# Kernel optimization log

Measured on AMD Instinct MI355X. Metric: run time of the kernel, lower is better.

## Reference

```python
import jax, jax.numpy as jnp
import numpy as np

# Dims: B=batch, C=n_car, N=n_node, E=embed_dim, H=n_heads
B, C, N, E = 64, 8, 512, 512
H = 8
CLIP = 10.0


def setup_inputs() -> dict:
    key = jax.random.key(0)
    ks = jax.random.split(key, 12)
    s = 1.0 / np.sqrt(E)
    mask = jax.random.bernoulli(ks[10], 0.3, (B, C, 1, N))
    mask = mask.at[..., 0].set(False)  # ensure at least one unmasked node per (b,c)
    return {
        "node_embeddings": jax.random.normal(ks[0], (B, N, E), jnp.float32),
        "graph_embedding": jax.random.normal(ks[1], (B, E), jnp.float32),
        "step_context": jax.random.normal(ks[2], (B, C, 1, E + 2), jnp.float32),
        "mask": mask,
        "Wk1": jax.random.normal(ks[3], (E, E), jnp.float32) * s,
        "Wv": jax.random.normal(ks[4], (E, E), jnp.float32) * s,
        "Wk2": jax.random.normal(ks[5], (E, E), jnp.float32) * s,
        "Wq_fixed": jax.random.normal(ks[6], (E, E), jnp.float32) * s,
        "Wout": jax.random.normal(ks[7], (E, E), jnp.float32) * s,
        "Wq_step": jax.random.normal(ks[8], (E, E + 2), jnp.float32) * s,
        "v": jax.random.uniform(ks[9], (E,), jnp.float32, -s, s),
    }


def reference(node_embeddings, graph_embedding, step_context, mask,
              Wk1, Wv, Wk2, Wq_fixed, Wout, Wq_step, v):
    dh = E // H
    neg = jnp.asarray(-1e9, node_embeddings.dtype)

    # compute_static: projections (torch Linear: x @ W.T). K/V/Q_fixed are
    # broadcast over the car dim instead of materialized via .repeat (same math).
    Q_fixed = (graph_embedding @ Wq_fixed.T)[:, None, None, :]  # [B,1,1,E]
    K1 = node_embeddings @ Wk1.T                                 # [B,N,E]
    V = node_embeddings @ Wv.T                                   # [B,N,E]
    K2 = node_embeddings @ Wk2.T                                 # [B,N,E]

    # compute_dynamic
    Q_step = step_context @ Wq_step.T                            # [B,C,1,E]
    Q1 = Q_fixed + Q_step                                        # [B,C,1,E]

    # MHA (need_W=False): split heads, masked scaled dot-product, merge heads.
    qh = Q1.reshape(B, C, H, dh)                                 # q-len 1 squeezed
    kh = K1.reshape(B, N, H, dh)
    vh = V.reshape(B, N, H, dh)
    scores = jnp.einsum('bchd,bnhd->bchn', qh, kh) * (1.0 / np.sqrt(dh))
    m = mask[:, :, 0, :][:, :, None, :]                          # [B,C,1,N]
    scores = jnp.where(m, neg, scores)
    attn = jax.nn.softmax(scores, axis=-1)
    heads = jnp.einsum('bchn,bnhd->bchd', attn, vh).reshape(B, C, E)
    Q3 = heads @ Wout.T                                          # [B,C,E] (Q2.squeeze(2))

    # Pointer logits (SHA): u = tanh(Q_fixed+Q_step) @ v, repeated over E,
    # dotted with K2 => u_scalar * sum_e K2, then tanh-clipped and masked.
    u_scalar = jnp.einsum('bcqe,e->bcq', jnp.tanh(Q1), v)        # [B,C,1]
    k2sum = K2.sum(-1)                                           # [B,N]
    raw = u_scalar * k2sum[:, None, :]                           # [B,C,N]
    logits = CLIP * jnp.tanh(raw * (1.0 / np.sqrt(E)))
    logits = jnp.where(mask[:, :, 0, :], neg, logits)
    logits = logits.reshape(B, C * N)                            # view(batch, -1)
    return logits, Q3
```

## Files before the change

kernel.cpp:

```cpp
#include <hip/hip_runtime.h>


typedef _Float16 f16x8 __attribute__((ext_vector_type(8)));
typedef float f32x4 __attribute__((ext_vector_type(4)));

__device__ __forceinline__ void async16(const void* g, void* l) {
  __builtin_amdgcn_global_load_lds(
      (const __attribute__((address_space(1))) unsigned int*)g,
      (__attribute__((address_space(3))) unsigned int*)l, 16, 0, 0);
}

__device__ __forceinline__ float fast_tanh(float x) {
  float ax = fabsf(x);
  float t = __expf(-2.f * ax);
  float r = (1.f - t) / (1.f + t);
  return copysignf(r, x);
}

__global__ __launch_bounds__(256) void prep_q1(
    const float* __restrict__ Wk1, const float* __restrict__ Wv,
    const float* __restrict__ Wk2, _Float16* __restrict__ W1h,
    _Float16* __restrict__ W2h, float* __restrict__ colsum,
    const float* __restrict__ ge, const float* __restrict__ sc,
    const float* __restrict__ Wqf, const float* __restrict__ Wqs,
    float* __restrict__ Q1) {
  const int bid = blockIdx.x;
  if (bid < 272) {
    if (bid < 16) {
      const int tx = threadIdx.x & 31, ty = threadIdx.x >> 5;
      const int col = bid * 32 + tx;
      float s = 0.f;
#pragma unroll 4
      for (int e = ty * 64; e < ty * 64 + 64; ++e) s += Wk2[e * 512 + col];
      __shared__ float red[8][32];
      red[ty][tx] = s;
      __syncthreads();
      if (ty == 0) {
        float t = 0.f;
#pragma unroll
        for (int g = 0; g < 8; ++g) t += red[g][tx];
        colsum[col] = t;
      }
    } else {
      const int cb = bid - 16;
      const float* src = (cb < 128) ? Wk1 : Wv;
      _Float16* dst = (cb < 128) ? W1h : W2h;
      const size_t off = (size_t)(cb & 127) * 2048 + threadIdx.x * 8;
      float4 a = *(const float4*)(src + off);
      float4 b = *(const float4*)(src + off + 4);
      union { _Float16 h[8]; uint4 u; } pk;
      pk.h[0] = (_Float16)a.x; pk.h[1] = (_Float16)a.y;
      pk.h[2] = (_Float16)a.z; pk.h[3] = (_Float16)a.w;
      pk.h[4] = (_Float16)b.x; pk.h[5] = (_Float16)b.y;
      pk.h[6] = (_Float16)b.z; pk.h[7] = (_Float16)b.w;
      *(uint4*)(dst + off) = pk.u;
    }
    return;
  }

  const int b2 = bid - 272;
  const int mb = b2 & 7, nb = (b2 >> 3) & 7, ks = b2 >> 6;
  const int tid = threadIdx.x;
  const int lane = tid & 63, wave = tid >> 6;
  const int wm = (wave >> 1) * 32, wn = (wave & 1) * 32;

  __shared__ __align__(16) _Float16 As[64][40];
  __shared__ __align__(16) _Float16 Ws[64][40];

  f32x4 acc[2][2] = {};
  const int qd = (lane >> 4) * 8, rr = lane & 15;

  for (int kt = 0; kt < 9; ++kt) {
    const int kb = ks * 288 + kt * 32;
#pragma unroll
    for (int f0 = 0; f0 < 2; ++f0) {
      int f = tid + f0 * 256;
      int r = f >> 3, c4 = (f & 7) * 4;
      int m = mb * 64 + r;
      int e = nb * 64 + r;
#pragma unroll
      for (int j = 0; j < 4; ++j) {
        int k = kb + c4 + j;
        float a = 0.f, w = 0.f;
        if (k < 512) {
          a = ge[(m >> 3) * 512 + k];
          w = Wqf[(size_t)e * 512 + k];
        } else if (k < 1026) {
          a = sc[(size_t)m * 514 + (k - 512)];
          w = Wqs[(size_t)e * 514 + (k - 512)];
        }
        As[r][c4 + j] = (_Float16)a;
        Ws[r][c4 + j] = (_Float16)w;
      }
    }
    __syncthreads();
    f16x8 af[2], bfr[2];
#pragma unroll
    for (int mi = 0; mi < 2; ++mi) af[mi] = *(const f16x8*)&As[wm + mi * 16 + rr][qd];
#pragma unroll
    for (int ni = 0; ni < 2; ++ni) bfr[ni] = *(const f16x8*)&Ws[wn + ni * 16 + rr][qd];
#pragma unroll
    for (int mi = 0; mi < 2; ++mi)
#pragma unroll
      for (int ni = 0; ni < 2; ++ni)
        acc[mi][ni] =
            __builtin_amdgcn_mfma_f32_16x16x32_f16(af[mi], bfr[ni], acc[mi][ni], 0, 0, 0);
    __syncthreads();
  }

  const int col = lane & 15, rq = (lane >> 4) * 4;
#pragma unroll
  for (int mi = 0; mi < 2; ++mi)
#pragma unroll
    for (int ni = 0; ni < 2; ++ni)
#pragma unroll
      for (int r = 0; r < 4; ++r) {
        int m = mb * 64 + wm + mi * 16 + rq + r;
        int e = nb * 64 + wn + ni * 16 + col;
        atomicAdd(&Q1[(size_t)m * 512 + e], acc[mi][ni][r]);
      }
}

__global__ __launch_bounds__(256, 2) void gemm_kv(
    const float* __restrict__ A, const _Float16* __restrict__ W1,
    const _Float16* __restrict__ W2, const float* __restrict__ colsum,
    _Float16* __restrict__ K1, _Float16* __restrict__ Vt,
    float* __restrict__ k2sum) {
  const int flat = (int)(blockIdx.y * 4 + blockIdx.x);
  const int work = (flat & 7) * 128 + (flat >> 3);
  const int nb = work & 3;
  const int mb = work >> 2;
  const int tid = threadIdx.x, lane = tid & 63, wave = tid >> 6;
  const int wm = (wave >> 1) * 64, wn = (wave & 1) * 64;
  const int row0 = mb * 128, col0 = nb * 128;
  const int b = mb >> 2;

  __shared__ __align__(16) _Float16 Ah[128 * 64];
  __shared__ __align__(16) _Float16 Wb[2][2][128 * 64];

  f32x4 acc1[4][4] = {}, acc2[4][4] = {};
  float k2p[4] = {0.f, 0.f, 0.f, 0.f};
  const int q = lane >> 4, rr = lane & 15;
  const int wlr = lane >> 3, wlc = lane & 7;
  const int cswz = wlc ^ wlr;

  const int ar0 = tid >> 3, ac = tid & 7;
  const float* aptr = A + (size_t)(row0 + ar0) * 512 + ac * 8;
  const int aslot = ac ^ (ar0 & 7);

  float4 areg[4][2];
  float4 cs0, cs1;

  auto issue_a = [&](int kt) {
#pragma unroll
    for (int j = 0; j < 4; ++j) {
      const float* gp = aptr + (size_t)j * 32 * 512 + kt * 64;
      areg[j][0] = *(const float4*)gp;
      areg[j][1] = *(const float4*)(gp + 4);
    }
    if (nb == 0) {
      const float* csp = colsum + kt * 64 + ac * 8;
      cs0 = *(const float4*)csp;
      cs1 = *(const float4*)(csp + 4);
    }
  };
  auto issue_w = [&](int kt, int buf) {
    const int kbase = kt * 64;
#pragma unroll
    for (int j = 0; j < 4; ++j) {
      int r = wave * 32 + j * 8 + wlr;
      int ldsrow = (wave * 32 + j * 8) * 64;
      size_t goff = (size_t)(col0 + r) * 512 + kbase + cswz * 8;
      async16(W1 + goff, &Wb[buf][0][ldsrow]);
      async16(W2 + goff, &Wb[buf][1][ldsrow]);
    }
  };
  auto write_a = [&](int kt) {
#pragma unroll
    for (int j = 0; j < 4; ++j) {
      union { _Float16 h[8]; uint4 u; } pk;
      float4 lo = areg[j][0], hi = areg[j][1];
      pk.h[0] = (_Float16)lo.x; pk.h[1] = (_Float16)lo.y;
      pk.h[2] = (_Float16)lo.z; pk.h[3] = (_Float16)lo.w;
      pk.h[4] = (_Float16)hi.x; pk.h[5] = (_Float16)hi.y;
      pk.h[6] = (_Float16)hi.z; pk.h[7] = (_Float16)hi.w;
      *(uint4*)&Ah[(ar0 + 32 * j) * 64 + aslot * 8] = pk.u;
    }
    if (nb == 0) {
#pragma unroll
      for (int j = 0; j < 4; ++j) {
        float4 lo = areg[j][0], hi = areg[j][1];
        k2p[j] += lo.x * cs0.x + lo.y * cs0.y + lo.z * cs0.z + lo.w * cs0.w +
                  hi.x * cs1.x + hi.y * cs1.y + hi.z * cs1.z + hi.w * cs1.w;
      }
    }
  };

  issue_a(0);
  issue_w(0, 0);
  write_a(0);
  __syncthreads();

  for (int kt = 0; kt < 8; ++kt) {
    const int p = kt & 1;
    if (kt < 7) {
      issue_a(kt + 1);
      issue_w(kt + 1, p ^ 1);
    }
#pragma unroll
    for (int k0 = 0; k0 < 64; k0 += 32) {
      const int cb = (k0 >> 3) + q;
      f16x8 af[4], b1[4], b2[4];
#pragma unroll
      for (int mi = 0; mi < 4; ++mi) {
        int ra = wm + mi * 16 + rr;
        af[mi] = *(const f16x8*)&Ah[ra * 64 + (cb ^ (ra & 7)) * 8];
      }
#pragma unroll
      for (int ni = 0; ni < 4; ++ni) {
        int rw = wn + ni * 16 + rr;
        int slot = cb ^ (rw & 7);
        b1[ni] = *(const f16x8*)&Wb[p][0][rw * 64 + slot * 8];
        b2[ni] = *(const f16x8*)&Wb[p][1][rw * 64 + slot * 8];
      }
      __builtin_amdgcn_s_setprio(1);
#pragma unroll
      for (int mi = 0; mi < 4; ++mi)
#pragma unroll
        for (int ni = 0; ni < 4; ++ni) {
          acc1[mi][ni] =
              __builtin_amdgcn_mfma_f32_16x16x32_f16(af[mi], b1[ni], acc1[mi][ni], 0, 0, 0);
          acc2[mi][ni] =
              __builtin_amdgcn_mfma_f32_16x16x32_f16(af[mi], b2[ni], acc2[mi][ni], 0, 0, 0);
        }
      __builtin_amdgcn_s_setprio(0);
    }
    if (kt < 7) {
      __syncthreads();
      write_a(kt + 1);
      __syncthreads();
    }
  }

  if (nb == 0) {
#pragma unroll
    for (int j = 0; j < 4; ++j) {
      float s = k2p[j];
      s += __shfl_xor(s, 1, 8);
      s += __shfl_xor(s, 2, 8);
      s += __shfl_xor(s, 4, 8);
      if (ac == 0) k2sum[row0 + (tid >> 3) + 32 * j] = s;
    }
  }

  const int col = lane & 15, rq = (lane >> 4) * 4;
#pragma unroll
  for (int mi = 0; mi < 4; ++mi)
#pragma unroll
    for (int ni = 0; ni < 4; ++ni)
#pragma unroll
      for (int r = 0; r < 4; ++r) {
        size_t m = row0 + wm + mi * 16 + rq + r;
        size_t e = col0 + wn + ni * 16 + col;
        K1[m * 512 + e] = (_Float16)acc1[mi][ni][r];
      }

  _Float16* Vts = &Wb[0][0][0];
#pragma unroll
  for (int mi = 0; mi < 4; ++mi)
#pragma unroll
    for (int ni = 0; ni < 4; ++ni) {
      int n0 = wm + mi * 16 + rq;
      int el = wn + ni * 16 + col;
      int cn = n0 >> 3, half = (n0 >> 2) & 1;
      int slot = cn ^ (el & 7);
      union { _Float16 h[4]; unsigned long long u; } pk;
#pragma unroll
      for (int r = 0; r < 4; ++r) pk.h[r] = (_Float16)acc2[mi][ni][r];
      *(unsigned long long*)&Vts[el * 128 + slot * 8 + half * 4] = pk.u;
    }
  __syncthreads();
  const int nbase = row0 & 511;
#pragma unroll
  for (int i = 0; i < 8; ++i) {
    int f = tid + i * 256;
    int el = f >> 4, c16 = f & 15;
    int slot = c16 ^ (el & 7);
    uint4 val = *(const uint4*)&Vts[el * 128 + slot * 8];
    *(uint4*)(Vt + (size_t)b * 262144 + (size_t)(col0 + el) * 512 + nbase + c16 * 8) = val;
  }
}

__global__ __launch_bounds__(256) void attn_kernel(
    const float* __restrict__ Q1, const _Float16* __restrict__ K1,
    const _Float16* __restrict__ Vt, const int* __restrict__ mask,
    float* __restrict__ heads) {
  const int bid = blockIdx.x;
  const int b = bid >> 3, h = bid & 7;
  const int tid = threadIdx.x, wave = tid >> 6, lane = tid & 63;
  const int q = lane >> 4, cl = lane & 15;

  __shared__ __align__(16) _Float16 kt[256 * 64];
  __shared__ __align__(16) _Float16 P[16][520];
  __shared__ float red[4][8];

  f16x8 af[2];
  {
    const float* qp = Q1 + (size_t)(b * 8 + (cl & 7)) * 512 + h * 64 + q * 8;
#pragma unroll
    for (int s = 0; s < 2; ++s) {
      float4 l0 = *(const float4*)(qp + s * 32);
      float4 l1 = *(const float4*)(qp + s * 32 + 4);
      af[s][0] = (_Float16)l0.x; af[s][1] = (_Float16)l0.y;
      af[s][2] = (_Float16)l0.z; af[s][3] = (_Float16)l0.w;
      af[s][4] = (_Float16)l1.x; af[s][5] = (_Float16)l1.y;
      af[s][6] = (_Float16)l1.z; af[s][7] = (_Float16)l1.w;
    }
  }

  f32x4 acc[8] = {};
  const _Float16* Kb = K1 + (size_t)b * 262144 + h * 64;
  for (int h2 = 0; h2 < 2; ++h2) {
#pragma unroll
    for (int j = 0; j < 8; ++j) {
      int r = wave * 64 + j * 8 + (lane >> 3);
      int cg = (lane & 7) ^ (r & 7);
      async16(Kb + (size_t)(h2 * 256 + r) * 512 + cg * 8, &kt[(wave * 64 + j * 8) * 64]);
    }
    __syncthreads();
    __builtin_amdgcn_s_setprio(1);
#pragma unroll
    for (int tt = 0; tt < 4; ++tt) {
      int rn = wave * 64 + tt * 16 + cl;
#pragma unroll
      for (int s = 0; s < 2; ++s) {
        int slot = (s * 4 + q) ^ (cl & 7);
        f16x8 bf = *(const f16x8*)&kt[rn * 64 + slot * 8];
        acc[h2 * 4 + tt] =
            __builtin_amdgcn_mfma_f32_16x16x32_f16(af[s], bf, acc[h2 * 4 + tt], 0, 0, 0);
      }
    }
    __builtin_amdgcn_s_setprio(0);
    __syncthreads();
  }

  const _Float16* Vb = Vt + (size_t)b * 262144 + (size_t)h * 64 * 512;
#pragma unroll
  for (int j = 0; j < 8; ++j) {
    int r = wave * 16 + j * 2 + (lane >> 5);
    int cg = (lane & 31) ^ (r & 7);
    async16(Vb + (size_t)r * 512 + cg * 8, &kt[(wave * 16 + j * 2) * 256]);
  }

  float gmax[4], rsum[4];
  if (q < 2) {
    float mx[4] = {-3e38f, -3e38f, -3e38f, -3e38f};
#pragma unroll
    for (int t = 0; t < 8; ++t) {
      int n = (t >> 2) * 256 + wave * 64 + (t & 3) * 16 + cl;
#pragma unroll
      for (int r = 0; r < 4; ++r) {
        int c = q * 4 + r;
        float x = mask[(size_t)(b * 8 + c) * 512 + n] ? -1e9f : acc[t][r] * 0.125f;
        acc[t][r] = x;
        mx[r] = fmaxf(mx[r], x);
      }
    }
#pragma unroll
    for (int off = 1; off < 16; off <<= 1)
#pragma unroll
      for (int r = 0; r < 4; ++r) mx[r] = fmaxf(mx[r], __shfl_xor(mx[r], off, 64));
    if (cl == 0)
#pragma unroll
      for (int r = 0; r < 4; ++r) red[wave][q * 4 + r] = mx[r];
  }
  __syncthreads();
  if (q < 2) {
#pragma unroll
    for (int r = 0; r < 4; ++r) {
      int c = q * 4 + r;
      gmax[r] = fmaxf(fmaxf(red[0][c], red[1][c]), fmaxf(red[2][c], red[3][c]));
    }
  }
  __syncthreads();
  if (q < 2) {
#pragma unroll
    for (int r = 0; r < 4; ++r) rsum[r] = 0.f;
#pragma unroll
    for (int t = 0; t < 8; ++t) {
      int n = (t >> 2) * 256 + wave * 64 + (t & 3) * 16 + cl;
#pragma unroll
      for (int r = 0; r < 4; ++r) {
        float e = __expf(acc[t][r] - gmax[r]);
        rsum[r] += e;
        P[q * 4 + r][n] = (_Float16)e;
      }
    }
#pragma unroll
    for (int off = 1; off < 16; off <<= 1)
#pragma unroll
      for (int r = 0; r < 4; ++r) rsum[r] += __shfl_xor(rsum[r], off, 64);
    if (cl == 0)
#pragma unroll
      for (int r = 0; r < 4; ++r) red[wave][q * 4 + r] = rsum[r];
  }
  __syncthreads();

  f32x4 pacc = {};
  const int rn = wave * 16 + cl;
  __builtin_amdgcn_s_setprio(1);
#pragma unroll
  for (int sl = 0; sl < 8; ++sl) {
    int slot = (sl * 4 + q) ^ (cl & 7);
    f16x8 bf = *(const f16x8*)&kt[rn * 256 + slot * 8];
    f16x8 pa = *(const f16x8*)&P[cl][sl * 32 + q * 8];
    pacc = __builtin_amdgcn_mfma_f32_16x16x32_f16(pa, bf, pacc, 0, 0, 0);
  }
  __builtin_amdgcn_s_setprio(0);
  __syncthreads();
#pragma unroll
  for (int j = 0; j < 8; ++j) {
    int r = wave * 16 + j * 2 + (lane >> 5);
    int cg = (lane & 31) ^ (r & 7);
    async16(Vb + (size_t)r * 512 + 256 + cg * 8, &kt[(wave * 16 + j * 2) * 256]);
  }
  __syncthreads();
  __builtin_amdgcn_s_setprio(1);
#pragma unroll
  for (int sl = 0; sl < 8; ++sl) {
    int slot = (sl * 4 + q) ^ (cl & 7);
    f16x8 bf = *(const f16x8*)&kt[rn * 256 + slot * 8];
    f16x8 pa = *(const f16x8*)&P[cl][256 + sl * 32 + q * 8];
    pacc = __builtin_amdgcn_mfma_f32_16x16x32_f16(pa, bf, pacc, 0, 0, 0);
  }
  __builtin_amdgcn_s_setprio(0);

  if (q < 2) {
#pragma unroll
    for (int r = 0; r < 4; ++r) {
      int c = q * 4 + r;
      float inv = 1.f / (red[0][c] + red[1][c] + red[2][c] + red[3][c]);
      heads[(size_t)(b * 8 + c) * 512 + h * 64 + wave * 16 + cl] = pacc[r] * inv;
    }
  }
}

__global__ __launch_bounds__(256) void out_logits(
    const float* __restrict__ A, const float* __restrict__ W,
    float* __restrict__ C, const float* __restrict__ Q1,
    const float* __restrict__ v, const float* __restrict__ k2s,
    const int* __restrict__ mask, float* __restrict__ out) {
  const int bid = blockIdx.x;
  if (bid < 256) {
    const int mb = bid & 7, nb = (bid >> 3) & 7, ks = bid >> 6;
    const int tid = threadIdx.x;
    const int lane = tid & 63, wave = tid >> 6;
    const int wm = (wave >> 1) * 32, wn = (wave & 1) * 32;

    __shared__ __align__(16) _Float16 As[64][40];
    __shared__ __align__(16) _Float16 Ws[64][40];

    f32x4 acc[2][2] = {};
    const int qd = (lane >> 4) * 8, rr = lane & 15;

    for (int kt = 0; kt < 4; ++kt) {
      const int kb = ks * 128 + kt * 32;
#pragma unroll
      for (int f0 = 0; f0 < 2; ++f0) {
        int f = tid + f0 * 256;
        int r = f >> 3, c4 = (f & 7) * 4;
        float4 a = *(const float4*)(A + (size_t)(mb * 64 + r) * 512 + kb + c4);
        float4 w = *(const float4*)(W + (size_t)(nb * 64 + r) * 512 + kb + c4);
        As[r][c4 + 0] = (_Float16)a.x; As[r][c4 + 1] = (_Float16)a.y;
        As[r][c4 + 2] = (_Float16)a.z; As[r][c4 + 3] = (_Float16)a.w;
        Ws[r][c4 + 0] = (_Float16)w.x; Ws[r][c4 + 1] = (_Float16)w.y;
        Ws[r][c4 + 2] = (_Float16)w.z; Ws[r][c4 + 3] = (_Float16)w.w;
      }
      __syncthreads();
      f16x8 af[2], bfr[2];
#pragma unroll
      for (int mi = 0; mi < 2; ++mi) af[mi] = *(const f16x8*)&As[wm + mi * 16 + rr][qd];
#pragma unroll
      for (int ni = 0; ni < 2; ++ni) bfr[ni] = *(const f16x8*)&Ws[wn + ni * 16 + rr][qd];
#pragma unroll
      for (int mi = 0; mi < 2; ++mi)
#pragma unroll
        for (int ni = 0; ni < 2; ++ni)
          acc[mi][ni] =
              __builtin_amdgcn_mfma_f32_16x16x32_f16(af[mi], bfr[ni], acc[mi][ni], 0, 0, 0);
      __syncthreads();
    }

    const int col = lane & 15, rq = (lane >> 4) * 4;
#pragma unroll
    for (int mi = 0; mi < 2; ++mi)
#pragma unroll
      for (int ni = 0; ni < 2; ++ni)
#pragma unroll
        for (int r = 0; r < 4; ++r) {
          int m = mb * 64 + wm + mi * 16 + rq + r;
          int e = nb * 64 + wn + ni * 16 + col;
          atomicAdd(&C[(size_t)m * 512 + e], acc[mi][ni][r]);
        }
    return;
  }

  const int bc = bid - 256;
  const int b = bc >> 3;
  const int tid = threadIdx.x;
  const int wave = tid >> 6, lane = tid & 63;

  float p = fast_tanh(Q1[(size_t)bc * 512 + tid]) * v[tid] +
            fast_tanh(Q1[(size_t)bc * 512 + tid + 256]) * v[tid + 256];
#pragma unroll
  for (int off = 32; off; off >>= 1) p += __shfl_down(p, off, 64);
  __shared__ float red[4];
  __shared__ float su;
  if (lane == 0) red[wave] = p;
  __syncthreads();
  if (tid == 0) su = red[0] + red[1] + red[2] + red[3];
  __syncthreads();
  const float u = su;

#pragma unroll
  for (int i = 0; i < 2; ++i) {
    int n = tid + i * 256;
    int idx = bc * 512 + n;
    out[idx] = mask[idx] ? -1e9f
                         : 10.f * fast_tanh(u * k2s[b * 512 + n] * 0.04419417382415922f);
  }
}

extern "C" void kernel_launch(void* const* d_in, const int* in_sizes, int n_in,
                              void* d_out, int out_size, void* d_ws, size_t ws_size,
                              hipStream_t stream) {
  const float* ne = (const float*)d_in[0];
  const float* ge = (const float*)d_in[1];
  const float* sc = (const float*)d_in[2];
  const int* mask = (const int*)d_in[3];
  const float* Wk1 = (const float*)d_in[4];
  const float* Wv = (const float*)d_in[5];
  const float* Wk2 = (const float*)d_in[6];
  const float* Wqf = (const float*)d_in[7];
  const float* Wout = (const float*)d_in[8];
  const float* Wqs = (const float*)d_in[9];
  const float* v = (const float*)d_in[10];

  float* logits = (float*)d_out;
  float* q3 = (float*)d_out + 262144;

  char* ws = (char*)d_ws;
  _Float16* K1 = (_Float16*)(ws + 0);
  _Float16* Vt = (_Float16*)(ws + 33554432);
  float* Q1 = (float*)(ws + 67108864);
  float* heads = (float*)(ws + 68157440);
  float* k2sum = (float*)(ws + 69206016);
  float* colsum = (float*)(ws + 69337088);
  _Float16* W1h = (_Float16*)(ws + 69339136);
  _Float16* W2h = (_Float16*)(ws + 69863424);

  hipMemsetAsync(Q1, 0, 1048576, stream);
  hipMemsetAsync(q3, 0, 1048576, stream);
  prep_q1<<<528, 256, 0, stream>>>(Wk1, Wv, Wk2, W1h, W2h, colsum,
                                   ge, sc, Wqf, Wqs, Q1);
  gemm_kv<<<dim3(4, 256), 256, 0, stream>>>(ne, W1h, W2h, colsum, K1, Vt, k2sum);
  attn_kernel<<<512, 256, 0, stream>>>(Q1, K1, Vt, mask, heads);
  out_logits<<<768, 256, 0, stream>>>(heads, Wout, q3, Q1, v, k2sum, mask, logits);
}
```

Measured before the change: 204.3 us.

## Fold Q1 projection into KV GEMM launch and drop split-K atomics

Moves the Q1 projection GEMM out of the weight-prep kernel and into the KV GEMM launch as 64 extra blocks that run over the full K range and use plain stores. The Wout GEMM gets the same treatment: split-K atomics are removed, so both memsets go away. The KV GEMM shared memory is recast as a single union buffer so both block roles can share it. The aim is to cut launches, memsets and atomic traffic. In exchange, each Q1/Q3 block now does a 4x longer serial K loop, with fewer blocks working in parallel.

```diff
diff --git a/kernel.cpp b/kernel.cpp
--- a/kernel.cpp
+++ b/kernel.cpp
@@ -17,126 +17,155 @@
   return copysignf(r, x);
 }
 
-__global__ __launch_bounds__(256) void prep_q1(
-    const float* __restrict__ Wk1, const float* __restrict__ Wv,
-    const float* __restrict__ Wk2, _Float16* __restrict__ W1h,
-    _Float16* __restrict__ W2h, float* __restrict__ colsum,
-    const float* __restrict__ ge, const float* __restrict__ sc,
-    const float* __restrict__ Wqf, const float* __restrict__ Wqs,
-    float* __restrict__ Q1) {
+__global__ __launch_bounds__(256) void prep_w(const float* __restrict__ Wk1,
+                                              const float* __restrict__ Wv,
+                                              const float* __restrict__ Wk2,
+                                              _Float16* __restrict__ W1h,
+                                              _Float16* __restrict__ W2h,
+                                              float* __restrict__ colsum) {
   const int bid = blockIdx.x;
-  if (bid < 272) {
-    if (bid < 16) {
-      const int tx = threadIdx.x & 31, ty = threadIdx.x >> 5;
-      const int col = bid * 32 + tx;
-      float s = 0.f;
+  if (bid < 16) {
+    const int tx = threadIdx.x & 31, ty = threadIdx.x >> 5;
+    const int col = bid * 32 + tx;
+    float s = 0.f;
 #pragma unroll 4
-      for (int e = ty * 64; e < ty * 64 + 64; ++e) s += Wk2[e * 512 + col];
-      __shared__ float red[8][32];
-      red[ty][tx] = s;
-      __syncthreads();
-      if (ty == 0) {
-        float t = 0.f;
-#pragma unroll
-        for (int g = 0; g < 8; ++g) t += red[g][tx];
-        colsum[col] = t;
-      }
-    } else {
-      const int cb = bid - 16;
-      const float* src = (cb < 128) ? Wk1 : Wv;
-      _Float16* dst = (cb < 128) ? W1h : W2h;
-      const size_t off = (size_t)(cb & 127) * 2048 + threadIdx.x * 8;
-      float4 a = *(const float4*)(src + off);
-      float4 b = *(const float4*)(src + off + 4);
-      union { _Float16 h[8]; uint4 u; } pk;
-      pk.h[0] = (_Float16)a.x; pk.h[1] = (_Float16)a.y;
-      pk.h[2] = (_Float16)a.z; pk.h[3] = (_Float16)a.w;
-      pk.h[4] = (_Float16)b.x; pk.h[5] = (_Float16)b.y;
-      pk.h[6] = (_Float16)b.z; pk.h[7] = (_Float16)b.w;
-      *(uint4*)(dst + off) = pk.u;
-    }
-    return;
-  }
-
-  const int b2 = bid - 272;
-  const int mb = b2 & 7, nb = (b2 >> 3) & 7, ks = b2 >> 6;
-  const int tid = threadIdx.x;
-  const int lane = tid & 63, wave = tid >> 6;
-  const int wm = (wave >> 1) * 32, wn = (wave & 1) * 32;
-
-  __shared__ __align__(16) _Float16 As[64][40];
-  __shared__ __align__(16) _Float16 Ws[64][40];
-
-  f32x4 acc[2][2] = {};
-  const int qd = (lane >> 4) * 8, rr = lane & 15;
-
-  for (int kt = 0; kt < 9; ++kt) {
-    const int kb = ks * 288 + kt * 32;
-#pragma unroll
-    for (int f0 = 0; f0 < 2; ++f0) {
-      int f = tid + f0 * 256;
-      int r = f >> 3, c4 = (f & 7) * 4;
-      int m = mb * 64 + r;
-      int e = nb * 64 + r;
-#pragma unroll
-      for (int j = 0; j < 4; ++j) {
-        int k = kb + c4 + j;
-        float a = 0.f, w = 0.f;
-        if (k < 512) {
-          a = ge[(m >> 3) * 512 + k];
-          w = Wqf[(size_t)e * 512 + k];
-        } else if (k < 1026) {
-          a = sc[(size_t)m * 514 + (k - 512)];
-          w = Wqs[(size_t)e * 514 + (k - 512)];
-        }
-        As[r][c4 + j] = (_Float16)a;
-        Ws[r][c4 + j] = (_Float16)w;
-      }
-    }
+    for (int e = ty * 64; e < ty * 64 + 64; ++e) s += Wk2[e * 512 + col];
+    __shared__ float red[8][32];
+    red[ty][tx] = s;
     __syncthreads();
-    f16x8 af[2], bfr[2];
-#pragma unroll
-    for (int mi = 0; mi < 2; ++mi) af[mi] = *(const f16x8*)&As[wm + mi * 16 + rr][qd];
-#pragma unroll
-    for (int ni = 0; ni < 2; ++ni) bfr[ni] = *(const f16x8*)&Ws[wn + ni * 16 + rr][qd];
-#pragma unroll
-    for (int mi = 0; mi < 2; ++mi)
-#pragma unroll
-      for (int ni = 0; ni < 2; ++ni)
-        acc[mi][ni] =
-            __builtin_amdgcn_mfma_f32_16x16x32_f16(af[mi], bfr[ni], acc[mi][ni], 0, 0, 0);
-    __syncthreads();
-  }
-
-  const int col = lane & 15, rq = (lane >> 4) * 4;
-#pragma unroll
-  for (int mi = 0; mi < 2; ++mi)
-#pragma unroll
-    for (int ni = 0; ni < 2; ++ni)
-#pragma unroll
-      for (int r = 0; r < 4; ++r) {
-        int m = mb * 64 + wm + mi * 16 + rq + r;
-        int e = nb * 64 + wn + ni * 16 + col;
-        atomicAdd(&Q1[(size_t)m * 512 + e], acc[mi][ni][r]);
-      }
-}
-
-__global__ __launch_bounds__(256, 2) void gemm_kv(
+    if (ty == 0) {
+      float t = 0.f;
+#pragma unroll
+      for (int g = 0; g < 8; ++g) t += red[g][tx];
+      colsum[col] = t;
+    }
+  } else {
+    const int cb = bid - 16;
+    const float* src = (cb < 128) ? Wk1 : Wv;
+    _Float16* dst = (cb < 128) ? W1h : W2h;
+    const size_t off = (size_t)(cb & 127) * 2048 + threadIdx.x * 8;
+    float4 a = *(const float4*)(src + off);
+    float4 b = *(const float4*)(src + off + 4);
+    union { _Float16 h[8]; uint4 u; } pk;
+    pk.h[0] = (_Float16)a.x; pk.h[1] = (_Float16)a.y;
+    pk.h[2] = (_Float16)a.z; pk.h[3] = (_Float16)a.w;
+    pk.h[4] = (_Float16)b.x; pk.h[5] = (_Float16)b.y;
+    pk.h[6] = (_Float16)b.z; pk.h[7] = (_Float16)b.w;
+    *(uint4*)(dst + off) = pk.u;
+  }
+}
+
+__global__ __launch_bounds__(256, 2) void kv_q1(
     const float* __restrict__ A, const _Float16* __restrict__ W1,
     const _Float16* __restrict__ W2, const float* __restrict__ colsum,
     _Float16* __restrict__ K1, _Float16* __restrict__ Vt,
-    float* __restrict__ k2sum) {
-  const int flat = (int)(blockIdx.y * 4 + blockIdx.x);
+    float* __restrict__ k2sum, const float* __restrict__ ge,
+    const float* __restrict__ sc, const float* __restrict__ Wqf,
+    const float* __restrict__ Wqs, float* __restrict__ Q1) {
+  __shared__ __align__(16) _Float16 S[40960];
+  const int bid = (int)blockIdx.x;
+  const int tid = threadIdx.x, lane = tid & 63, wave = tid >> 6;
+
+  if (bid < 64) {
+    const int mb = bid & 7, nb = bid >> 3;
+    const int wm = (wave >> 1) * 32, wn = (wave & 1) * 32;
+    _Float16(*As)[40] = (_Float16(*)[40])S;
+    _Float16(*Ws)[40] = (_Float16(*)[40])(S + 2560);
+
+    f32x4 acc[2][2] = {};
+    const int qd = (lane >> 4) * 8, rr = lane & 15;
+    const int r = tid >> 3, c4 = (tid & 7) * 4;
+    const int r1 = (tid + 256) >> 3;
+    const int m = mb * 64 + r, e = nb * 64 + r;
+    const int m1 = mb * 64 + r1, e1 = nb * 64 + r1;
+
+    for (int kt = 0; kt < 16; ++kt) {
+      const int kb = kt * 32;
+      {
+        float4 a = *(const float4*)(ge + (size_t)(m >> 3) * 512 + kb + c4);
+        float4 w = *(const float4*)(Wqf + (size_t)e * 512 + kb + c4);
+        As[r][c4 + 0] = (_Float16)a.x; As[r][c4 + 1] = (_Float16)a.y;
+        As[r][c4 + 2] = (_Float16)a.z; As[r][c4 + 3] = (_Float16)a.w;
+        Ws[r][c4 + 0] = (_Float16)w.x; Ws[r][c4 + 1] = (_Float16)w.y;
+        Ws[r][c4 + 2] = (_Float16)w.z; Ws[r][c4 + 3] = (_Float16)w.w;
+        a = *(const float4*)(ge + (size_t)(m1 >> 3) * 512 + kb + c4);
+        w = *(const float4*)(Wqf + (size_t)e1 * 512 + kb + c4);
+        As[r1][c4 + 0] = (_Float16)a.x; As[r1][c4 + 1] = (_Float16)a.y;
+        As[r1][c4 + 2] = (_Float16)a.z; As[r1][c4 + 3] = (_Float16)a.w;
+        Ws[r1][c4 + 0] = (_Float16)w.x; Ws[r1][c4 + 1] = (_Float16)w.y;
+        Ws[r1][c4 + 2] = (_Float16)w.z; Ws[r1][c4 + 3] = (_Float16)w.w;
+      }
+      __syncthreads();
+      f16x8 af[2], bfr[2];
+#pragma unroll
+      for (int mi = 0; mi < 2; ++mi) af[mi] = *(const f16x8*)&As[wm + mi * 16 + rr][qd];
+#pragma unroll
+      for (int ni = 0; ni < 2; ++ni) bfr[ni] = *(const f16x8*)&Ws[wn + ni * 16 + rr][qd];
+#pragma unroll
+      for (int mi = 0; mi < 2; ++mi)
+#pragma unroll
+        for (int ni = 0; ni < 2; ++ni)
+          acc[mi][ni] =
+              __builtin_amdgcn_mfma_f32_16x16x32_f16(af[mi], bfr[ni], acc[mi][ni], 0, 0, 0);
+      __syncthreads();
+    }
+    for (int kt = 16; kt < 36; ++kt) {
+      const int kb = kt * 32;
+#pragma unroll
+      for (int f0 = 0; f0 < 2; ++f0) {
+        int rr2 = f0 ? r1 : r;
+        int mm = mb * 64 + rr2, ee = nb * 64 + rr2;
+#pragma unroll
+        for (int j = 0; j < 4; ++j) {
+          int k = kb + c4 + j - 512;
+          float a = 0.f, w = 0.f;
+          if (k < 514) {
+            a = sc[(size_t)mm * 514 + k];
+            w = Wqs[(size_t)ee * 514 + k];
+          }
+          As[rr2][c4 + j] = (_Float16)a;
+          Ws[rr2][c4 + j] = (_Float16)w;
+        }
+      }
+      __syncthreads();
+      f16x8 af[2], bfr[2];
+#pragma unroll
+      for (int mi = 0; mi < 2; ++mi) af[mi] = *(const f16x8*)&As[wm + mi * 16 + rr][qd];
+#pragma unroll
+      for (int ni = 0; ni < 2; ++ni) bfr[ni] = *(const f16x8*)&Ws[wn + ni * 16 + rr][qd];
+#pragma unroll
+      for (int mi = 0; mi < 2; ++mi)
+#pragma unroll
+        for (int ni = 0; ni < 2; ++ni)
+          acc[mi][ni] =
+              __builtin_amdgcn_mfma_f32_16x16x32_f16(af[mi], bfr[ni], acc[mi][ni], 0, 0, 0);
+      __syncthreads();
+    }
+
+    const int col = lane & 15, rq = (lane >> 4) * 4;
+#pragma unroll
+    for (int mi = 0; mi < 2; ++mi)
+#pragma unroll
+      for (int ni = 0; ni < 2; ++ni)
+#pragma unroll
+        for (int rj = 0; rj < 4; ++rj) {
+          int mm = mb * 64 + wm + mi * 16 + rq + rj;
+          int ee = nb * 64 + wn + ni * 16 + col;
+          Q1[(size_t)mm * 512 + ee] = acc[mi][ni][rj];
+        }
+    return;
+  }
+
+  const int flat = bid - 64;
   const int work = (flat & 7) * 128 + (flat >> 3);
   const int nb = work & 3;
   const int mb = work >> 2;
-  const int tid = threadIdx.x, lane = tid & 63, wave = tid >> 6;
   const int wm = (wave >> 1) * 64, wn = (wave & 1) * 64;
   const int row0 = mb * 128, col0 = nb * 128;
   const int b = mb >> 2;
 
-  __shared__ __align__(16) _Float16 Ah[128 * 64];
-  __shared__ __align__(16) _Float16 Wb[2][2][128 * 64];
+  _Float16* Ah = S;
+  _Float16* WbP = S + 8192;
 
   f32x4 acc1[4][4] = {}, acc2[4][4] = {};
   float k2p[4] = {0.f, 0.f, 0.f, 0.f};
@@ -171,8 +200,8 @@
       int r = wave * 32 + j * 8 + wlr;
       int ldsrow = (wave * 32 + j * 8) * 64;
       size_t goff = (size_t)(col0 + r) * 512 + kbase + cswz * 8;
-      async16(W1 + goff, &Wb[buf][0][ldsrow]);
-      async16(W2 + goff, &Wb[buf][1][ldsrow]);
+      async16(W1 + goff, WbP + buf * 16384 + ldsrow);
+      async16(W2 + goff, WbP + buf * 16384 + 8192 + ldsrow);
     }
   };
   auto write_a = [&](int kt) {
@@ -220,8 +249,8 @@
       for (int ni = 0; ni < 4; ++ni) {
         int rw = wn + ni * 16 + rr;
         int slot = cb ^ (rw & 7);
-        b1[ni] = *(const f16x8*)&Wb[p][0][rw * 64 + slot * 8];
-        b2[ni] = *(const f16x8*)&Wb[p][1][rw * 64 + slot * 8];
+        b1[ni] = *(const f16x8*)&WbP[p * 16384 + rw * 64 + slot * 8];
+        b2[ni] = *(const f16x8*)&WbP[p * 16384 + 8192 + rw * 64 + slot * 8];
       }
       __builtin_amdgcn_s_setprio(1);
 #pragma unroll
@@ -249,7 +278,7 @@
       s += __shfl_xor(s, 1, 8);
       s += __shfl_xor(s, 2, 8);
       s += __shfl_xor(s, 4, 8);
-      if (ac == 0) k2sum[row0 + (tid >> 3) + 32 * j] = s;
+      if (ac == 0) k2sum[row0 + ar0 + 32 * j] = s;
     }
   }
 
@@ -265,7 +294,7 @@
         K1[m * 512 + e] = (_Float16)acc1[mi][ni][r];
       }
 
-  _Float16* Vts = &Wb[0][0][0];
+  _Float16* Vts = WbP;
 #pragma unroll
   for (int mi = 0; mi < 4; ++mi)
 #pragma unroll
@@ -451,8 +480,8 @@
     const float* __restrict__ v, const float* __restrict__ k2s,
     const int* __restrict__ mask, float* __restrict__ out) {
   const int bid = blockIdx.x;
-  if (bid < 256) {
-    const int mb = bid & 7, nb = (bid >> 3) & 7, ks = bid >> 6;
+  if (bid < 64) {
+    const int mb = bid & 7, nb = bid >> 3;
     const int tid = threadIdx.x;
     const int lane = tid & 63, wave = tid >> 6;
     const int wm = (wave >> 1) * 32, wn = (wave & 1) * 32;
@@ -463,8 +492,8 @@
     f32x4 acc[2][2] = {};
     const int qd = (lane >> 4) * 8, rr = lane & 15;
 
-    for (int kt = 0; kt < 4; ++kt) {
-      const int kb = ks * 128 + kt * 32;
+    for (int kt = 0; kt < 16; ++kt) {
+      const int kb = kt * 32;
 #pragma unroll
       for (int f0 = 0; f0 < 2; ++f0) {
         int f = tid + f0 * 256;
@@ -500,12 +529,12 @@
         for (int r = 0; r < 4; ++r) {
           int m = mb * 64 + wm + mi * 16 + rq + r;
           int e = nb * 64 + wn + ni * 16 + col;
-          atomicAdd(&C[(size_t)m * 512 + e], acc[mi][ni][r]);
+          C[(size_t)m * 512 + e] = acc[mi][ni][r];
         }
     return;
   }
 
-  const int bc = bid - 256;
+  const int bc = bid - 64;
   const int b = bc >> 3;
   const int tid = threadIdx.x;
   const int wave = tid >> 6, lane = tid & 63;
@@ -559,11 +588,9 @@
   _Float16* W1h = (_Float16*)(ws + 69339136);
   _Float16* W2h = (_Float16*)(ws + 69863424);
 
-  hipMemsetAsync(Q1, 0, 1048576, stream);
-  hipMemsetAsync(q3, 0, 1048576, stream);
-  prep_q1<<<528, 256, 0, stream>>>(Wk1, Wv, Wk2, W1h, W2h, colsum,
-                                   ge, sc, Wqf, Wqs, Q1);
-  gemm_kv<<<dim3(4, 256), 256, 0, stream>>>(ne, W1h, W2h, colsum, K1, Vt, k2sum);
+  prep_w<<<272, 256, 0, stream>>>(Wk1, Wv, Wk2, W1h, W2h, colsum);
+  kv_q1<<<1088, 256, 0, stream>>>(ne, W1h, W2h, colsum, K1, Vt, k2sum,
+                                  ge, sc, Wqf, Wqs, Q1);
   attn_kernel<<<512, 256, 0, stream>>>(Q1, K1, Vt, mask, heads);
-  out_logits<<<768, 256, 0, stream>>>(heads, Wout, q3, Q1, v, k2sum, mask, logits);
-}
+  out_logits<<<576, 256, 0, stream>>>(heads, Wout, q3, Q1, v, k2sum, mask, logits);
+}
```

Result: slower. 215.2 us (+5.4%).
